# Kernel optimization log

Measured on AMD Instinct MI355X. Metric: run time of the kernel, lower is better.

Reference implementation:

```python
import jax, jax.numpy as jnp
import numpy as np

B, T, D, H = 4, 2048, 1024, 16
HD = D // H  # head_size = 64
EPS = 1e-5


def layernorm(x, g, b):
    mu = jnp.mean(x, axis=-1, keepdims=True)
    var = jnp.var(x, axis=-1, keepdims=True)
    return (x - mu) * jax.lax.rsqrt(var + EPS) * g + b


def setup_inputs() -> dict:
    key = jax.random.key(0)
    ks = jax.random.split(key, 8)
    s = 0.02
    return {
        "x": jax.random.normal(ks[0], (B, T, D), jnp.float32),
        "Wq": jax.random.normal(ks[1], (D, D), jnp.float32) * s,
        "Wk": jax.random.normal(ks[2], (D, D), jnp.float32) * s,
        "Wv": jax.random.normal(ks[3], (D, D), jnp.float32) * s,
        "Wo": jax.random.normal(ks[4], (D, D), jnp.float32) * s,
        "bo": jnp.zeros((D,), jnp.float32),
        "W1": jax.random.normal(ks[5], (D, 4 * D), jnp.float32) * s,
        "b1": jnp.zeros((4 * D,), jnp.float32),
        "W2": jax.random.normal(ks[6], (4 * D, D), jnp.float32) * s,
        "b2": jnp.zeros((D,), jnp.float32),
        "ln1_g": jnp.ones((D,), jnp.float32),
        "ln1_b": jnp.zeros((D,), jnp.float32),
        "ln2_g": jnp.ones((D,), jnp.float32),
        "ln2_b": jnp.zeros((D,), jnp.float32),
    }


def reference(x, Wq, Wk, Wv, Wo, bo, W1, b1, W2, b2, ln1_g, ln1_b, ln2_g, ln2_b):
    # --- multi-head causal self-attention (pre-LN), dropout off (eval) ---
    h = layernorm(x, ln1_g, ln1_b)
    q = jnp.einsum('btd,de->bte', h, Wq).reshape(B, T, H, HD)
    k = jnp.einsum('btd,de->bte', h, Wk).reshape(B, T, H, HD)
    v = jnp.einsum('btd,de->bte', h, Wv).reshape(B, T, H, HD)
    scores = jnp.einsum('bqhd,bkhd->bhqk', q, k) * (HD ** -0.5)
    causal = jnp.tril(jnp.ones((T, T), bool))
    scores = jnp.where(causal, scores, -jnp.inf)
    attn = jax.nn.softmax(scores, axis=-1)
    out = jnp.einsum('bhqk,bkhd->bqhd', attn, v).reshape(B, T, D)
    out = jnp.einsum('btd,de->bte', out, Wo) + bo
    x = x + out
    # --- feed-forward: Linear -> ReLU -> Linear -> ReLU (as in source) ---
    h2 = layernorm(x, ln2_g, ln2_b)
    ff = jax.nn.relu(jnp.einsum('btd,df->btf', h2, W1) + b1)
    ff = jax.nn.relu(jnp.einsum('btf,fd->btd', ff, W2) + b2)
    return x + ff
```

## Files before the change

### kernel.cpp

```cpp
#include <hip/hip_runtime.h>
#include <cstdint>
#include <cstddef>

typedef unsigned short u16;
typedef __attribute__((ext_vector_type(8))) short bf16x8;
typedef __attribute__((ext_vector_type(4))) float f32x4;
typedef __attribute__((address_space(1))) const unsigned int gu32;
typedef __attribute__((address_space(3))) unsigned int lu32;

#define QSCALE 0.1803368801111204f

__device__ __forceinline__ u16 f2bf(float f) {
  uint32_t u = __float_as_uint(f);
  u += 0x7fffu + ((u >> 16) & 1u);
  return (u16)(u >> 16);
}

__device__ __forceinline__ void xcd_swz(int& bn, int& bm) {
  int gx = (int)gridDim.x;
  int n = gx * (int)gridDim.y;
  int lid = (int)blockIdx.x + gx * (int)blockIdx.y;
  int nid = (lid & 7) * (n >> 3) + (lid >> 3);
  bn = nid % gx;
  bm = nid / gx;
}

__global__ __launch_bounds__(256) void transpose_w(const float* __restrict__ W,
                                                   u16* __restrict__ WT,
                                                   int K, int N) {
  __shared__ float t[32][33];
  int n0 = blockIdx.x * 32, k0 = blockIdx.y * 32;
  for (int i = threadIdx.y; i < 32; i += 8)
    t[i][threadIdx.x] = W[(size_t)(k0 + i) * N + n0 + threadIdx.x];
  __syncthreads();
  for (int i = threadIdx.y; i < 32; i += 8)
    WT[(size_t)(n0 + i) * K + k0 + threadIdx.x] = f2bf(t[threadIdx.x][i]);
}

__global__ __launch_bounds__(256) void ln_kernel(const float* __restrict__ x,
                                                 const float* __restrict__ g,
                                                 const float* __restrict__ b,
                                                 u16* __restrict__ out) {
  int row = blockIdx.x;
  const float4 v = *(const float4*)(x + (size_t)row * 1024 + threadIdx.x * 4);
  float s = v.x + v.y + v.z + v.w;
  float ss = v.x * v.x + v.y * v.y + v.z * v.z + v.w * v.w;
#pragma unroll
  for (int d = 1; d < 64; d <<= 1) { s += __shfl_xor(s, d); ss += __shfl_xor(ss, d); }
  __shared__ float rs_[4], rss_[4];
  int wv = threadIdx.x >> 6;
  if ((threadIdx.x & 63) == 0) { rs_[wv] = s; rss_[wv] = ss; }
  __syncthreads();
  s = rs_[0] + rs_[1] + rs_[2] + rs_[3];
  ss = rss_[0] + rss_[1] + rss_[2] + rss_[3];
  float mu = s * (1.f / 1024.f);
  float var = ss * (1.f / 1024.f) - mu * mu;
  float rstd = rsqrtf(var + 1e-5f);
  float4 gv = *(const float4*)(g + threadIdx.x * 4);
  float4 bv = *(const float4*)(b + threadIdx.x * 4);
  uint32_t lo = (uint32_t)f2bf((v.x - mu) * rstd * gv.x + bv.x) |
                ((uint32_t)f2bf((v.y - mu) * rstd * gv.y + bv.y) << 16);
  uint32_t hi = (uint32_t)f2bf((v.z - mu) * rstd * gv.z + bv.z) |
                ((uint32_t)f2bf((v.w - mu) * rstd * gv.w + bv.w) << 16);
  uint2 o; o.x = lo; o.y = hi;
  *(uint2*)(out + (size_t)row * 1024 + threadIdx.x * 4) = o;
}

#define STAGEA(slot, tnext, is)                                               \
  __builtin_amdgcn_global_load_lds(                                           \
      (gu32*)((const char*)(A + (size_t)(bm * 256 + (is) * 64 + srow) * K +   \
                            (size_t)(tnext) * 64) + ssw),                     \
      (lu32*)&lds[(slot) * 24576 + (is) * 4096 + wid * 512], 16, 0, 0)
#define STAGEB(slot, tnext, is)                                               \
  __builtin_amdgcn_global_load_lds(                                           \
      (gu32*)((const char*)(BT + (size_t)(bn * 128 + (is) * 64 + srow) * K +  \
                            (size_t)(tnext) * 64) + ssw),                     \
      (lu32*)&lds[(slot) * 24576 + 16384 + (is) * 4096 + wid * 512], 16, 0, 0)

template <int MODE>
__global__ __launch_bounds__(512, 2) void gemm8p(
    const u16* __restrict__ A, const u16* __restrict__ BT,
    int M, int N, int K,
    const float* __restrict__ bias, const float* __restrict__ resid,
    float* __restrict__ outf,
    u16* __restrict__ ob0, u16* __restrict__ ob1, u16* __restrict__ ob2) {
  __shared__ __align__(16) u16 lds[73728];
  const int tid = threadIdx.x, lane = tid & 63, wid = tid >> 6;
  const int wr = wid >> 1, wc = wid & 1;
  int bn, bm;
  xcd_swz(bn, bm);
  const int l15 = lane & 15, lhi = lane >> 4;
  const int srow = tid >> 3;
  const int ssw = ((tid & 7) * 16) ^ ((srow & 7) << 4);
  const int cs0 = (lhi * 8) ^ ((l15 & 7) << 3);
  const int cs1 = (32 + lhi * 8) ^ ((l15 & 7) << 3);
  const int arow = (wr * 64 + l15) * 64;
  const int brow = (wc * 64 + l15) * 64;

  f32x4 acc[4][4];
#pragma unroll
  for (int i = 0; i < 4; ++i)
#pragma unroll
    for (int j = 0; j < 4; ++j) acc[i][j] = (f32x4){0.f, 0.f, 0.f, 0.f};

  const int NT = K >> 6;

#pragma unroll
  for (int t0 = 0; t0 < 2; ++t0) {
    STAGEA(t0, t0, 0); STAGEA(t0, t0, 1); STAGEA(t0, t0, 2); STAGEA(t0, t0, 3);
    STAGEB(t0, t0, 0); STAGEB(t0, t0, 1);
  }
  asm volatile("s_waitcnt vmcnt(6)" ::: "memory");
  __builtin_amdgcn_s_barrier();

  int s = 0, sn = 2;
  for (int t = 0; t < NT; ++t) {
    const bool hasPre = (t + 2) < NT;
    const int aoff = s * 24576, boff = s * 24576 + 16384;

    bf16x8 bfr[4][2], afr[2][2];
#pragma unroll
    for (int ni = 0; ni < 4; ++ni) {
      bfr[ni][0] = *(const bf16x8*)&lds[boff + brow + ni * 1024 + cs0];
      bfr[ni][1] = *(const bf16x8*)&lds[boff + brow + ni * 1024 + cs1];
    }
    afr[0][0] = *(const bf16x8*)&lds[aoff + arow + cs0];
    afr[0][1] = *(const bf16x8*)&lds[aoff + arow + cs1];
    afr[1][0] = *(const bf16x8*)&lds[aoff + arow + 1024 + cs0];
    afr[1][1] = *(const bf16x8*)&lds[aoff + arow + 1024 + cs1];
    if (hasPre) { STAGEA(sn, t + 2, 0); STAGEA(sn, t + 2, 1); STAGEB(sn, t + 2, 0); }
    __builtin_amdgcn_s_barrier();
    __builtin_amdgcn_s_setprio(1);
#pragma unroll
    for (int ks = 0; ks < 2; ++ks)
#pragma unroll
      for (int ml = 0; ml < 2; ++ml)
#pragma unroll
        for (int ni = 0; ni < 4; ++ni)
          acc[ml][ni] = __builtin_amdgcn_mfma_f32_16x16x32_bf16(afr[ml][ks], bfr[ni][ks], acc[ml][ni], 0, 0, 0);
    __builtin_amdgcn_s_setprio(0);
    __builtin_amdgcn_s_barrier();

    afr[0][0] = *(const bf16x8*)&lds[aoff + arow + 2048 + cs0];
    afr[0][1] = *(const bf16x8*)&lds[aoff + arow + 2048 + cs1];
    afr[1][0] = *(const bf16x8*)&lds[aoff + arow + 3072 + cs0];
    afr[1][1] = *(const bf16x8*)&lds[aoff + arow + 3072 + cs1];
    if (hasPre) { STAGEA(sn, t + 2, 2); STAGEA(sn, t + 2, 3); STAGEB(sn, t + 2, 1); }
    __builtin_amdgcn_s_barrier();
    __builtin_amdgcn_s_setprio(1);
#pragma unroll
    for (int ks = 0; ks < 2; ++ks)
#pragma unroll
      for (int ml = 0; ml < 2; ++ml)
#pragma unroll
        for (int ni = 0; ni < 4; ++ni)
          acc[2 + ml][ni] = __builtin_amdgcn_mfma_f32_16x16x32_bf16(afr[ml][ks], bfr[ni][ks], acc[2 + ml][ni], 0, 0, 0);
    __builtin_amdgcn_s_setprio(0);
    if (hasPre) {
      asm volatile("s_waitcnt vmcnt(6)" ::: "memory");
    } else if (t + 1 < NT) {
      asm volatile("s_waitcnt vmcnt(0)" ::: "memory");
    }
    __builtin_amdgcn_s_barrier();

    s = (s == 2) ? 0 : s + 1;
    sn = (sn == 2) ? 0 : sn + 1;
  }

  if (MODE == 0) {
    char* ep = (char*)lds;
    const bool vmode = (bn >= 16);
    if (vmode) {
#pragma unroll
      for (int mi = 0; mi < 4; ++mi)
#pragma unroll
        for (int ni = 0; ni < 4; ++ni) {
          uint32_t lo, hi;
          asm("v_cvt_pk_bf16_f32 %0, %1, %2"
              : "=v"(lo) : "v"(acc[mi][ni][0]), "v"(acc[mi][ni][1]));
          asm("v_cvt_pk_bf16_f32 %0, %1, %2"
              : "=v"(hi) : "v"(acc[mi][ni][2]), "v"(acc[mi][ni][3]));
          uint2 pk; pk.x = lo; pk.y = hi;
          int c_local = wc * 64 + ni * 16 + l15;
          int rb = wr * 64 + mi * 16 + lhi * 4;
          *(uint2*)(ep + c_local * 528 + rb * 2) = pk;
        }
    } else {
      const float sc = (bn < 8) ? QSCALE : 1.f;
#pragma unroll
      for (int mi = 0; mi < 4; ++mi)
#pragma unroll
        for (int ni = 0; ni < 4; ++ni) {
          int c_local = wc * 64 + ni * 16 + l15;
          int rb = wr * 64 + mi * 16 + lhi * 4;
#pragma unroll
          for (int r = 0; r < 4; ++r) {
            *(u16*)(ep + (rb + r) * 272 + c_local * 2) = f2bf(acc[mi][ni][r] * sc);
          }
        }
    }
    __syncthreads();
    if (vmode) {
#pragma unroll
      for (int i = 0; i < 8; ++i) {
        int idx = i * 512 + tid;
        int c = idx >> 5, tc = idx & 31;
        uint4 d4 = *(const uint4*)(ep + c * 528 + tc * 16);
        int cm = bn * 128 + c - 2048, hh = cm >> 6, dd = cm & 63;
        size_t bh = (size_t)((bm >> 3) * 16 + hh);
        int t0 = (bm & 7) * 256;
        *(uint4*)&ob2[(bh * 64 + dd) * 2048 + t0 + tc * 8] = d4;
      }
    } else {
#pragma unroll
      for (int i = 0; i < 8; ++i) {
        int idx = i * 512 + tid;
        int row = idx >> 4, cc = idx & 15;
        uint4 d4 = *(const uint4*)(ep + row * 272 + cc * 16);
        size_t rg = (size_t)(bm * 256 + row);
        int colg = bn * 128 + cc * 8;
        if (colg < 1024)
          *(uint4*)&ob0[rg * 1024 + colg] = d4;
        else
          *(uint4*)&ob1[rg * 1024 + colg - 1024] = d4;
      }
    }
  } else {
    float* epf = (float*)lds;
#pragma unroll
    for (int h = 0; h < 2; ++h) {
      __syncthreads();
      if ((wr >> 1) == h) {
#pragma unroll
        for (int mi = 0; mi < 4; ++mi)
#pragma unroll
          for (int ni = 0; ni < 4; ++ni) {
            int c_local = wc * 64 + ni * 16 + l15;
            int rl = (wr & 1) * 64 + mi * 16 + lhi * 4;
#pragma unroll
            for (int r = 0; r < 4; ++r)
              epf[(rl + r) * 132 + c_local] = acc[mi][ni][r];
          }
      }
      __syncthreads();
#pragma unroll
      for (int i = 0; i < 8; ++i) {
        int idx = i * 512 + tid;
        int row = idx >> 5, cc = idx & 31;
        float4 v = *(const float4*)&epf[row * 132 + cc * 4];
        int colg = bn * 128 + cc * 4;
        size_t rg = (size_t)(bm * 256 + h * 128 + row);
        float4 bv = *(const float4*)&bias[colg];
        float4 rv = *(const float4*)&resid[rg * (size_t)N + colg];
        float4 o4;
        if (MODE == 1) {
          o4.x = v.x + bv.x + rv.x; o4.y = v.y + bv.y + rv.y;
          o4.z = v.z + bv.z + rv.z; o4.w = v.w + bv.w + rv.w;
        } else {
          o4.x = fmaxf(v.x + bv.x, 0.f) + rv.x;
          o4.y = fmaxf(v.y + bv.y, 0.f) + rv.y;
          o4.z = fmaxf(v.z + bv.z, 0.f) + rv.z;
          o4.w = fmaxf(v.w + bv.w, 0.f) + rv.w;
        }
        *(float4*)&outf[rg * (size_t)N + colg] = o4;
      }
    }
  }
}

#define SA32(slot, t, inst)                                                   \
  __builtin_amdgcn_global_load_lds(                                           \
      (gu32*)((const char*)(A + (size_t)(bm * 256 + (inst) * 128 +            \
                            (tid >> 2)) * K + (size_t)(t) * 32) + ssw2),      \
      (lu32*)&lds[(slot) * 16384 + (inst) * 4096 + tid * 8], 16, 0, 0)
#define SB32(slot, t, inst)                                                   \
  __builtin_amdgcn_global_load_lds(                                           \
      (gu32*)((const char*)(BT + (size_t)(bn * 256 + (inst) * 128 +           \
                            (tid >> 2)) * K + (size_t)(t) * 32) + ssw2),      \
      (lu32*)&lds[(slot) * 16384 + 8192 + (inst) * 4096 + tid * 8], 16, 0, 0)
#define STAGE32(slot, t)                                                      \
  do { SA32(slot, t, 0); SA32(slot, t, 1); SB32(slot, t, 0); SB32(slot, t, 1); } while (0)

__global__ __launch_bounds__(512, 2) void gemm256p(
    const u16* __restrict__ A, const u16* __restrict__ BT,
    int M, int N, int K,
    const float* __restrict__ bias, u16* __restrict__ out) {
  __shared__ __align__(16) u16 lds[65536];
  const int tid = threadIdx.x, lane = tid & 63, wid = tid >> 6;
  const int wr = wid >> 2, wc = wid & 3;
  int bn, bm;
  xcd_swz(bn, bm);
  const int l15 = lane & 15, lhi = lane >> 4;
  const int ssw2 = ((tid & 3) * 16) ^ (((tid >> 3) & 3) << 4);
  const int cb = (lhi * 16) ^ (((l15 >> 1) & 3) << 4);

  f32x4 acc[8][4];
#pragma unroll
  for (int i = 0; i < 8; ++i)
#pragma unroll
    for (int j = 0; j < 4; ++j) acc[i][j] = (f32x4){0.f, 0.f, 0.f, 0.f};

  const int NT = K >> 5;

  STAGE32(0, 0); STAGE32(1, 1); STAGE32(2, 2);
  asm volatile("s_waitcnt vmcnt(8)" ::: "memory");
  __builtin_amdgcn_s_barrier();

  bf16x8 bfr0[4], afr0[4], bfr1[4], afr1[4], afr2[4];
  {
    const char* Ap = (const char*)lds;
    const char* Bp = Ap + 16384;
#pragma unroll
    for (int nf = 0; nf < 4; ++nf)
      bfr0[nf] = *(const bf16x8*)(Bp + (wc * 64 + nf * 16 + l15) * 64 + cb);
#pragma unroll
    for (int mf = 0; mf < 4; ++mf)
      afr0[mf] = *(const bf16x8*)(Ap + (wr * 128 + mf * 16 + l15) * 64 + cb);
  }

#define BODY32(t, bfrC, afrC, bfrN, afrN)                                      \
  {                                                                            \
    const char* Ap = (const char*)lds + (size_t)((t) & 3) * 32768;             \
    if ((t) + 3 < NT) STAGE32(((t) + 3) & 3, (t) + 3);                         \
    _Pragma("unroll")                                                          \
    for (int mf = 0; mf < 4; ++mf)                                             \
      afr2[mf] = *(const bf16x8*)(Ap + (wr * 128 + (4 + mf) * 16 + l15) * 64 + cb); \
    __builtin_amdgcn_s_setprio(1);                                             \
    _Pragma("unroll")                                                          \
    for (int mf = 0; mf < 4; ++mf)                                             \
      _Pragma("unroll")                                                        \
      for (int nf = 0; nf < 4; ++nf)                                           \
        acc[mf][nf] = __builtin_amdgcn_mfma_f32_16x16x32_bf16(afrC[mf], bfrC[nf], acc[mf][nf], 0, 0, 0); \
    __builtin_amdgcn_s_setprio(0);                                             \
    if ((t) + 3 < NT)      asm volatile("s_waitcnt vmcnt(8)" ::: "memory");    \
    else if ((t) + 2 < NT) asm volatile("s_waitcnt vmcnt(4)" ::: "memory");    \
    else if ((t) + 1 < NT) asm volatile("s_waitcnt vmcnt(0)" ::: "memory");    \
    __builtin_amdgcn_s_barrier();                                              \
    if ((t) + 1 < NT) {                                                        \
      const char* Apn = (const char*)lds + (size_t)(((t) + 1) & 3) * 32768;    \
      const char* Bpn = Apn + 16384;                                           \
      _Pragma("unroll")                                                        \
      for (int nf = 0; nf < 4; ++nf)                                           \
        bfrN[nf] = *(const bf16x8*)(Bpn + (wc * 64 + nf * 16 + l15) * 64 + cb); \
      _Pragma("unroll")                                                        \
      for (int mf = 0; mf < 4; ++mf)                                           \
        afrN[mf] = *(const bf16x8*)(Apn + (wr * 128 + mf * 16 + l15) * 64 + cb); \
    }                                                                          \
    __builtin_amdgcn_s_setprio(1);                                             \
    _Pragma("unroll")                                                          \
    for (int mf = 0; mf < 4; ++mf)                                             \
      _Pragma("unroll")                                                        \
      for (int nf = 0; nf < 4; ++nf)                                           \
        acc[4 + mf][nf] = __builtin_amdgcn_mfma_f32_16x16x32_bf16(afr2[mf], bfrC[nf], acc[4 + mf][nf], 0, 0, 0); \
    __builtin_amdgcn_s_setprio(0);                                             \
  }

  for (int tt = 0; tt < NT; tt += 2) {
    BODY32(tt, bfr0, afr0, bfr1, afr1);
    BODY32(tt + 1, bfr1, afr1, bfr0, afr0);
  }
#undef BODY32

  char* ep = (char*)lds;
#pragma unroll
  for (int h = 0; h < 2; ++h) {
    __syncthreads();
    if (wr == h) {
#pragma unroll
      for (int ni = 0; ni < 4; ++ni) {
        int c_local = wc * 64 + ni * 16 + l15;
        float bv = bias[bn * 256 + c_local];
#pragma unroll
        for (int mi = 0; mi < 8; ++mi) {
          int rb = mi * 16 + lhi * 4;
#pragma unroll
          for (int r = 0; r < 4; ++r) {
            float v = fmaxf(acc[mi][ni][r] + bv, 0.f);
            *(u16*)(ep + (rb + r) * 528 + c_local * 2) = f2bf(v);
          }
        }
      }
    }
    __syncthreads();
#pragma unroll
    for (int i = 0; i < 8; ++i) {
      int idx = i * 512 + tid;
      int row = idx >> 5, cc = idx & 31;
      uint4 d4 = *(const uint4*)(ep + row * 528 + cc * 16);
      size_t rg = (size_t)(bm * 256 + h * 128 + row);
      *(uint4*)&out[rg * (size_t)N + bn * 256 + cc * 8] = d4;
    }
  }
}

__global__ __launch_bounds__(512) void attn_kernel(
    const u16* __restrict__ Qb, const u16* __restrict__ Kb,
    const u16* __restrict__ VTb, u16* __restrict__ O) {
  const int p = blockIdx.x;
  const int bh = blockIdx.y;
  const int b = bh >> 4, h = bh & 15;
  const u16* Q = Qb + (size_t)b * 2048 * 1024 + h * 64;
  const u16* Kn = Kb + (size_t)b * 2048 * 1024 + h * 64;
  const u16* VT = VTb + (size_t)bh * 64 * 2048;
  const int tid = threadIdx.x, lane = tid & 63, wv = tid >> 6;
  const int l15 = lane & 15, lhi = lane >> 4;
  const int srow = tid >> 3;
  const int scol16 = (tid & 7) * 16;
  const int sw = scol16 ^ ((srow & 7) << 4);
  const int rswz = (l15 & 7) << 4;
  const int cb0 = (lhi * 16) ^ rswz;
  const int cb1 = (64 + lhi * 16) ^ rswz;

  __shared__ __align__(16) u16 KV[2][2][4096];
  __shared__ u16 Ps[8][16 * 72];

#define STAGEKV(slot, kt)                                                     \
  do {                                                                        \
    __builtin_amdgcn_global_load_lds(                                         \
        (gu32*)((const char*)(Kn + (size_t)((kt)*64 + srow) * 1024) + sw),    \
        (lu32*)&KV[slot][0][wv * 512], 16, 0, 0);                             \
    __builtin_amdgcn_global_load_lds(                                         \
        (gu32*)((const char*)(VT + (size_t)srow * 2048 + (kt)*64) + sw),      \
        (lu32*)&KV[slot][1][wv * 512], 16, 0, 0);                             \
  } while (0)

#pragma unroll
  for (int pass = 0; pass < 2; ++pass) {
    const int chunk = pass ? p : (15 - p);
    const int qbase = chunk * 128 + wv * 16;
    const int nkt = 2 * chunk + 2;

    bf16x8 qf[2];
#pragma unroll
    for (int ks = 0; ks < 2; ++ks)
      qf[ks] = *(const bf16x8*)&Q[(size_t)(qbase + l15) * 1024 + ks * 32 + lhi * 8];

    f32x4 o[4];
#pragma unroll
    for (int f = 0; f < 4; ++f) o[f] = (f32x4){0.f, 0.f, 0.f, 0.f};
    float m = -1e30f;
    float l = 0.f;

    __syncthreads();
    STAGEKV(0, 0);

    for (int kt = 0; kt < nkt; ++kt) {
      const int cs = kt & 1;
      asm volatile("s_waitcnt vmcnt(0)" ::: "memory");
      __syncthreads();
      if (kt + 1 < nkt) STAGEKV(cs ^ 1, kt + 1);

      if (kt * 64 <= qbase + 15) {
        const char* Kbase = (const char*)&KV[cs][0][0];
        const char* Vbase = (const char*)&KV[cs][1][0];

        f32x4 s[4];
#pragma unroll
        for (int jt = 0; jt < 4; ++jt) s[jt] = (f32x4){0.f, 0.f, 0.f, 0.f};
        __builtin_amdgcn_s_setprio(1);
#pragma unroll
        for (int ks = 0; ks < 2; ++ks) {
          const int cbyte = ks ? cb1 : cb0;
#pragma unroll
          for (int jt = 0; jt < 4; ++jt) {
            bf16x8 kf = *(const bf16x8*)(Kbase + (jt * 16 + l15) * 128 + cbyte);
            s[jt] = __builtin_amdgcn_mfma_f32_16x16x32_bf16(kf, qf[ks], s[jt], 0, 0, 0);
          }
        }
        __builtin_amdgcn_s_setprio(0);

        if (kt * 64 + 63 > qbase) {
          int qg = qbase + l15;
#pragma unroll
          for (int jt = 0; jt < 4; ++jt)
#pragma unroll
            for (int r = 0; r < 4; ++r) {
              int kg = kt * 64 + jt * 16 + lhi * 4 + r;
              if (kg > qg) s[jt][r] = -1e30f;
            }
        }

        float mr = fmaxf(fmaxf(s[0][0], s[0][1]), fmaxf(s[0][2], s[0][3]));
#pragma unroll
        for (int jt = 1; jt < 4; ++jt)
          mr = fmaxf(mr, fmaxf(fmaxf(s[jt][0], s[jt][1]), fmaxf(s[jt][2], s[jt][3])));
        mr = fmaxf(mr, __shfl_xor(mr, 16));
        mr = fmaxf(mr, __shfl_xor(mr, 32));
        if (__any(mr > m + 8.f)) {
          float mn = fmaxf(m, mr);
          float sc = exp2f(m - mn);
          l *= sc;
          m = mn;
#pragma unroll
          for (int r = 0; r < 4; ++r) {
            float so = __shfl(sc, lhi * 4 + r);
#pragma unroll
            for (int f = 0; f < 4; ++f) o[f][r] *= so;
          }
        }

        float rs = 0.f;
#pragma unroll
        for (int jt = 0; jt < 4; ++jt)
#pragma unroll
          for (int r = 0; r < 4; ++r) {
            float pv = exp2f(s[jt][r] - m);
            s[jt][r] = pv;
            rs += pv;
          }
        rs += __shfl_xor(rs, 16);
        rs += __shfl_xor(rs, 32);
        l += rs;

#pragma unroll
        for (int jt = 0; jt < 4; ++jt) {
          uint32_t lo, hi;
          asm("v_cvt_pk_bf16_f32 %0, %1, %2"
              : "=v"(lo) : "v"(s[jt][0]), "v"(s[jt][1]));
          asm("v_cvt_pk_bf16_f32 %0, %1, %2"
              : "=v"(hi) : "v"(s[jt][2]), "v"(s[jt][3]));
          uint2 pk; pk.x = lo; pk.y = hi;
          *(uint2*)&Ps[wv][l15 * 72 + jt * 16 + lhi * 4] = pk;
        }
        __builtin_amdgcn_s_setprio(1);
#pragma unroll
        for (int ks = 0; ks < 2; ++ks) {
          const int cbyte = ks ? cb1 : cb0;
          bf16x8 pf = *(const bf16x8*)&Ps[wv][l15 * 72 + ks * 32 + lhi * 8];
#pragma unroll
          for (int f = 0; f < 4; ++f) {
            bf16x8 vfr = *(const bf16x8*)(Vbase + (f * 16 + l15) * 128 + cbyte);
            o[f] = __builtin_amdgcn_mfma_f32_16x16x32_bf16(pf, vfr, o[f], 0, 0, 0);
          }
        }
        __builtin_amdgcn_s_setprio(0);
      }
    }

#pragma unroll
    for (int r = 0; r < 4; ++r) {
      float ld = __shfl(l, lhi * 4 + r);
      float inv = 1.f / ld;
      int t = qbase + lhi * 4 + r;
#pragma unroll
      for (int f = 0; f < 4; ++f)
        O[((size_t)(b * 2048 + t)) * 1024 + h * 64 + f * 16 + l15] = f2bf(o[f][r] * inv);
    }
  }
#undef STAGEKV
}

extern "C" void kernel_launch(void* const* d_in, const int* in_sizes, int n_in,
                              void* d_out, int out_size, void* d_ws, size_t ws_size,
                              hipStream_t stream) {
  const float* x   = (const float*)d_in[0];
  const float* Wq  = (const float*)d_in[1];
  const float* Wk  = (const float*)d_in[2];
  const float* Wv  = (const float*)d_in[3];
  const float* Wo  = (const float*)d_in[4];
  const float* bo  = (const float*)d_in[5];
  const float* W1  = (const float*)d_in[6];
  const float* b1  = (const float*)d_in[7];
  const float* W2  = (const float*)d_in[8];
  const float* b2  = (const float*)d_in[9];
  const float* g1  = (const float*)d_in[10];
  const float* be1 = (const float*)d_in[11];
  const float* g2  = (const float*)d_in[12];
  const float* be2 = (const float*)d_in[13];

  char* p = (char*)d_ws;
  auto alloc = [&](size_t bytes) {
    char* r = p;
    p += (bytes + 255) & ~(size_t)255;
    return r;
  };
  u16* WqkvT = (u16*)alloc(3072ull * 1024 * 2);
  u16* WoT   = (u16*)alloc(1024ull * 1024 * 2);
  u16* W1T   = (u16*)alloc(4096ull * 1024 * 2);
  u16* W2T   = (u16*)alloc(1024ull * 4096 * 2);
  u16* hln   = (u16*)alloc(8192ull * 1024 * 2);
  u16* Qbuf  = (u16*)alloc(8192ull * 1024 * 2);
  u16* Kbuf  = (u16*)alloc(8192ull * 1024 * 2);
  u16* VTbuf = (u16*)alloc(8192ull * 1024 * 2);
  float* x2  = (float*)alloc(8192ull * 1024 * 4);
  u16* ff1   = (u16*)alloc(8192ull * 4096 * 2);
  u16* Oattn = hln;
  u16* h2    = Qbuf;
  if ((size_t)(p - (char*)d_ws) > ws_size) return;

  dim3 tb(32, 8);
  transpose_w<<<dim3(32, 32), tb, 0, stream>>>(Wq, WqkvT, 1024, 1024);
  transpose_w<<<dim3(32, 32), tb, 0, stream>>>(Wk, WqkvT + 1024 * 1024, 1024, 1024);
  transpose_w<<<dim3(32, 32), tb, 0, stream>>>(Wv, WqkvT + 2048 * 1024, 1024, 1024);
  transpose_w<<<dim3(32, 32), tb, 0, stream>>>(Wo, WoT, 1024, 1024);
  transpose_w<<<dim3(128, 32), tb, 0, stream>>>(W1, W1T, 1024, 4096);
  transpose_w<<<dim3(32, 128), tb, 0, stream>>>(W2, W2T, 4096, 1024);

  ln_kernel<<<8192, 256, 0, stream>>>(x, g1, be1, hln);

  gemm8p<0><<<dim3(24, 32), 512, 0, stream>>>(hln, WqkvT, 8192, 3072, 1024,
                                              nullptr, nullptr, nullptr,
                                              Qbuf, Kbuf, VTbuf);

  attn_kernel<<<dim3(8, 64), 512, 0, stream>>>(Qbuf, Kbuf, VTbuf, Oattn);

  gemm8p<1><<<dim3(8, 32), 512, 0, stream>>>(Oattn, WoT, 8192, 1024, 1024,
                                             bo, x, x2, nullptr, nullptr, nullptr);

  ln_kernel<<<8192, 256, 0, stream>>>(x2, g2, be2, h2);

  gemm256p<<<dim3(16, 32), 512, 0, stream>>>(h2, W1T, 8192, 4096, 1024, b1, ff1);

  gemm8p<3><<<dim3(8, 32), 512, 0, stream>>>(ff1, W2T, 8192, 1024, 4096,
                                             b2, x2, (float*)d_out, nullptr, nullptr, nullptr);
}
```

Before: 393.9 us.

## Restructure FFN1 GEMM main loop into four barrier-separated phases

Replaces the register double-buffered, two-step unrolled main loop of the W1 GEMM with a single-step loop. Each iteration splits the global-to-LDS prefetch into A and B halves and places them in separate phases between LDS fragment reads and MFMA blocks, with a barrier after each phase. The goal is to interleave memory issue with MFMA work across waves in a ping-pong style. In exchange it drops the cross-iteration prefetch of the next fragments into registers and adds four barriers per K step, which could expose LDS read latency.

New measurement: 390.1 us. About the same (-1.0%).

```diff
diff --git a/kernel.cpp b/kernel.cpp
--- a/kernel.cpp
+++ b/kernel.cpp
@@ -278,10 +278,8 @@
       (gu32*)((const char*)(BT + (size_t)(bn * 256 + (inst) * 128 +           \
                             (tid >> 2)) * K + (size_t)(t) * 32) + ssw2),      \
       (lu32*)&lds[(slot) * 16384 + 8192 + (inst) * 4096 + tid * 8], 16, 0, 0)
-#define STAGE32(slot, t)                                                      \
-  do { SA32(slot, t, 0); SA32(slot, t, 1); SB32(slot, t, 0); SB32(slot, t, 1); } while (0)
-
-__global__ __launch_bounds__(512, 2) void gemm256p(
+
+__global__ __launch_bounds__(512, 2) void gemm_m201(
     const u16* __restrict__ A, const u16* __restrict__ BT,
     int M, int N, int K,
     const float* __restrict__ bias, u16* __restrict__ out) {
@@ -302,64 +300,54 @@
 
   const int NT = K >> 5;
 
-  STAGE32(0, 0); STAGE32(1, 1); STAGE32(2, 2);
+#pragma unroll
+  for (int s0 = 0; s0 < 3; ++s0) {
+    SA32(s0, s0, 0); SA32(s0, s0, 1); SB32(s0, s0, 0); SB32(s0, s0, 1);
+  }
   asm volatile("s_waitcnt vmcnt(8)" ::: "memory");
   __builtin_amdgcn_s_barrier();
 
-  bf16x8 bfr0[4], afr0[4], bfr1[4], afr1[4], afr2[4];
-  {
-    const char* Ap = (const char*)lds;
+  for (int t = 0; t < NT; ++t) {
+    const char* Ap = (const char*)lds + (size_t)(t & 3) * 32768;
     const char* Bp = Ap + 16384;
+    const int sl = (t + 3) & 3;
+
+    if (t + 3 < NT) { SA32(sl, t + 3, 0); SA32(sl, t + 3, 1); }
+    bf16x8 bfr[4], afr[4];
 #pragma unroll
     for (int nf = 0; nf < 4; ++nf)
-      bfr0[nf] = *(const bf16x8*)(Bp + (wc * 64 + nf * 16 + l15) * 64 + cb);
+      bfr[nf] = *(const bf16x8*)(Bp + (wc * 64 + nf * 16 + l15) * 64 + cb);
 #pragma unroll
     for (int mf = 0; mf < 4; ++mf)
-      afr0[mf] = *(const bf16x8*)(Ap + (wr * 128 + mf * 16 + l15) * 64 + cb);
+      afr[mf] = *(const bf16x8*)(Ap + (wr * 128 + mf * 16 + l15) * 64 + cb);
+    __builtin_amdgcn_s_barrier();
+    __builtin_amdgcn_s_setprio(1);
+#pragma unroll
+    for (int mf = 0; mf < 4; ++mf)
+#pragma unroll
+      for (int nf = 0; nf < 4; ++nf)
+        acc[mf][nf] = __builtin_amdgcn_mfma_f32_16x16x32_bf16(afr[mf], bfr[nf], acc[mf][nf], 0, 0, 0);
+    __builtin_amdgcn_s_setprio(0);
+    __builtin_amdgcn_s_barrier();
+
+    if (t + 3 < NT) { SB32(sl, t + 3, 0); SB32(sl, t + 3, 1); }
+    bf16x8 afr2[4];
+#pragma unroll
+    for (int mf = 0; mf < 4; ++mf)
+      afr2[mf] = *(const bf16x8*)(Ap + (wr * 128 + (4 + mf) * 16 + l15) * 64 + cb);
+    if (t + 3 < NT)      asm volatile("s_waitcnt vmcnt(8)" ::: "memory");
+    else if (t + 2 < NT) asm volatile("s_waitcnt vmcnt(4)" ::: "memory");
+    else if (t + 1 < NT) asm volatile("s_waitcnt vmcnt(0)" ::: "memory");
+    __builtin_amdgcn_s_barrier();
+    __builtin_amdgcn_s_setprio(1);
+#pragma unroll
+    for (int mf = 0; mf < 4; ++mf)
+#pragma unroll
+      for (int nf = 0; nf < 4; ++nf)
+        acc[4 + mf][nf] = __builtin_amdgcn_mfma_f32_16x16x32_bf16(afr2[mf], bfr[nf], acc[4 + mf][nf], 0, 0, 0);
+    __builtin_amdgcn_s_setprio(0);
+    __builtin_amdgcn_s_barrier();
   }
-
-#define BODY32(t, bfrC, afrC, bfrN, afrN)                                      \
-  {                                                                            \
-    const char* Ap = (const char*)lds + (size_t)((t) & 3) * 32768;             \
-    if ((t) + 3 < NT) STAGE32(((t) + 3) & 3, (t) + 3);                         \
-    _Pragma("unroll")                                                          \
-    for (int mf = 0; mf < 4; ++mf)                                             \
-      afr2[mf] = *(const bf16x8*)(Ap + (wr * 128 + (4 + mf) * 16 + l15) * 64 + cb); \
-    __builtin_amdgcn_s_setprio(1);                                             \
-    _Pragma("unroll")                                                          \
-    for (int mf = 0; mf < 4; ++mf)                                             \
-      _Pragma("unroll")                                                        \
-      for (int nf = 0; nf < 4; ++nf)                                           \
-        acc[mf][nf] = __builtin_amdgcn_mfma_f32_16x16x32_bf16(afrC[mf], bfrC[nf], acc[mf][nf], 0, 0, 0); \
-    __builtin_amdgcn_s_setprio(0);                                             \
-    if ((t) + 3 < NT)      asm volatile("s_waitcnt vmcnt(8)" ::: "memory");    \
-    else if ((t) + 2 < NT) asm volatile("s_waitcnt vmcnt(4)" ::: "memory");    \
-    else if ((t) + 1 < NT) asm volatile("s_waitcnt vmcnt(0)" ::: "memory");    \
-    __builtin_amdgcn_s_barrier();                                              \
-    if ((t) + 1 < NT) {                                                        \
-      const char* Apn = (const char*)lds + (size_t)(((t) + 1) & 3) * 32768;    \
-      const char* Bpn = Apn + 16384;                                           \
-      _Pragma("unroll")                                                        \
-      for (int nf = 0; nf < 4; ++nf)                                           \
-        bfrN[nf] = *(const bf16x8*)(Bpn + (wc * 64 + nf * 16 + l15) * 64 + cb); \
-      _Pragma("unroll")                                                        \
-      for (int mf = 0; mf < 4; ++mf)                                           \
-        afrN[mf] = *(const bf16x8*)(Apn + (wr * 128 + mf * 16 + l15) * 64 + cb); \
-    }                                                                          \
-    __builtin_amdgcn_s_setprio(1);                                             \
-    _Pragma("unroll")                                                          \
-    for (int mf = 0; mf < 4; ++mf)                                             \
-      _Pragma("unroll")                                                        \
-      for (int nf = 0; nf < 4; ++nf)                                           \
-        acc[4 + mf][nf] = __builtin_amdgcn_mfma_f32_16x16x32_bf16(afr2[mf], bfrC[nf], acc[4 + mf][nf], 0, 0, 0); \
-    __builtin_amdgcn_s_setprio(0);                                             \
-  }
-
-  for (int tt = 0; tt < NT; tt += 2) {
-    BODY32(tt, bfr0, afr0, bfr1, afr1);
-    BODY32(tt + 1, bfr1, afr1, bfr0, afr0);
-  }
-#undef BODY32
 
   char* ep = (char*)lds;
 #pragma unroll
@@ -609,7 +597,7 @@
 
   ln_kernel<<<8192, 256, 0, stream>>>(x2, g2, be2, h2);
 
-  gemm256p<<<dim3(16, 32), 512, 0, stream>>>(h2, W1T, 8192, 4096, 1024, b1, ff1);
+  gemm_m201<<<dim3(16, 32), 512, 0, stream>>>(h2, W1T, 8192, 4096, 1024, b1, ff1);
 
   gemm8p<3><<<dim3(8, 32), 512, 0, stream>>>(ff1, W2T, 8192, 1024, 4096,
                                              b2, x2, (float*)d_out, nullptr, nullptr, nullptr);
```
